# Kernel tuning notes

Hardware: AMD Instinct MI355X
Metric: run time of the kernel (lower is better)

## Reference

```python
import jax, jax.numpy as jnp
import numpy as np

N_NODES = 50000
N_EDGES = 500000
IN_DIM = 128
HIDDEN = 32
HEADS = 8
OUT_DIM = HIDDEN * HEADS  # 256
NEG_SLOPE = 0.2


def setup_inputs() -> dict:
    key = jax.random.key(0)
    ks = jax.random.split(key, 10)
    s = lambda fan: 1.0 / np.sqrt(fan)
    x = jax.random.normal(ks[0], (N_NODES, IN_DIM), dtype=jnp.float32)
    edge_index = jax.random.randint(ks[1], (2, N_EDGES), 0, N_NODES, dtype=jnp.int32)
    W1 = jax.random.normal(ks[2], (IN_DIM, HEADS * HIDDEN), jnp.float32) * s(IN_DIM)
    a_src1 = jax.random.normal(ks[3], (HEADS, HIDDEN), jnp.float32) * s(HIDDEN)
    a_dst1 = jax.random.normal(ks[4], (HEADS, HIDDEN), jnp.float32) * s(HIDDEN)
    b1 = jnp.zeros((HEADS * HIDDEN,), jnp.float32)
    W2 = jax.random.normal(ks[5], (OUT_DIM, OUT_DIM), jnp.float32) * s(OUT_DIM)
    a_src2 = jax.random.normal(ks[6], (1, OUT_DIM), jnp.float32) * s(OUT_DIM)
    a_dst2 = jax.random.normal(ks[7], (1, OUT_DIM), jnp.float32) * s(OUT_DIM)
    b2 = jnp.zeros((OUT_DIM,), jnp.float32)
    return {"x": x, "edge_index": edge_index, "W1": W1, "a_src1": a_src1,
            "a_dst1": a_dst1, "b1": b1, "W2": W2, "a_src2": a_src2,
            "a_dst2": a_dst2, "b2": b2}


def _gat_layer(x, src, dst, W, a_src, a_dst, b, heads, ch, concat):
    N = x.shape[0]
    h = (x @ W).reshape(N, heads, ch)                      # [N,H,C]
    e_src = jnp.sum(h * a_src[None], axis=-1)              # [N,H]
    e_dst = jnp.sum(h * a_dst[None], axis=-1)              # [N,H]
    e = jax.nn.leaky_relu(e_src[src] + e_dst[dst], NEG_SLOPE)  # [E,H]
    # softmax over incoming edges of each destination node
    m = jax.ops.segment_max(e, dst, num_segments=N)        # [N,H]
    e = jnp.exp(e - m[dst])
    denom = jax.ops.segment_sum(e, dst, num_segments=N)    # [N,H]
    alpha = e / (denom[dst] + 1e-16)                       # [E,H]
    msg = h[src] * alpha[:, :, None]                       # [E,H,C]
    out = jax.ops.segment_sum(msg, dst, num_segments=N)    # [N,H,C]
    out = out.reshape(N, heads * ch) if concat else out.mean(axis=1)
    return out + b


def reference(x, edge_index, W1, a_src1, a_dst1, b1, W2, a_src2, a_dst2, b2):
    N = x.shape[0]
    # add self loops (PyG GATConv default)
    loops = jnp.arange(N, dtype=edge_index.dtype)
    src = jnp.concatenate([edge_index[0], loops])
    dst = jnp.concatenate([edge_index[1], loops])
    # dropout is identity in eval mode
    h = _gat_layer(x, src, dst, W1, a_src1, a_dst1, b1, HEADS, HIDDEN, True)
    h = jax.nn.elu(h)
    out = _gat_layer(h, src, dst, W2, a_src2, a_dst2, b2, 1, OUT_DIM, False)
    return out
```

## Files before the change

kernel.cpp:

```cpp
#include <hip/hip_runtime.h>
#include <math.h>

#define N_NODES 50000
#define E_ORIG  500000
#define E_TOT   550000
#define NB      196

typedef _Float16 half8 __attribute__((ext_vector_type(8)));
typedef _Float16 half4 __attribute__((ext_vector_type(4)));
typedef float    v4f   __attribute__((ext_vector_type(4)));

__global__ void k_zero(int* __restrict__ p, int n) {
    int i = blockIdx.x * blockDim.x + threadIdx.x;
    if (i < n) p[i] = 0;
}

__global__ void k_count(const int* __restrict__ ei, int* __restrict__ deg) {
    int e = blockIdx.x * blockDim.x + threadIdx.x;
    if (e >= E_TOT) return;
    int d = (e < E_ORIG) ? ei[E_ORIG + e] : (e - E_ORIG);
    atomicAdd(&deg[d], 1);
}

__global__ __launch_bounds__(256) void k_blocksum(const int* __restrict__ deg,
                                                  int* __restrict__ bsum) {
    int t = threadIdx.x;
    int i = blockIdx.x * 256 + t;
    int v = (i < N_NODES) ? deg[i] : 0;
#pragma unroll
    for (int mk = 1; mk < 64; mk <<= 1) v += __shfl_xor(v, mk, 64);
    __shared__ int ws[4];
    if ((t & 63) == 0) ws[t >> 6] = v;
    __syncthreads();
    if (t == 0) bsum[blockIdx.x] = ws[0] + ws[1] + ws[2] + ws[3];
}

__global__ __launch_bounds__(256) void k_scanbsum(const int* __restrict__ bsum,
                                                  int* __restrict__ boff) {
    __shared__ int s[256];
    int t = threadIdx.x;
    int v = (t < NB) ? bsum[t] : 0;
    s[t] = v;
    __syncthreads();
    for (int o = 1; o < 256; o <<= 1) {
        int x = (t >= o) ? s[t - o] : 0;
        __syncthreads();
        s[t] += x;
        __syncthreads();
    }
    if (t <= NB) boff[t] = (t == 0) ? 0 : s[t - 1];
}

__global__ __launch_bounds__(256) void k_offsets(const int* __restrict__ deg,
                                                 const int* __restrict__ boff,
                                                 int* __restrict__ offsets,
                                                 int* __restrict__ cur) {
    __shared__ int s[256];
    int t = threadIdx.x;
    int i = blockIdx.x * 256 + t;
    int v = (i < N_NODES) ? deg[i] : 0;
    s[t] = v;
    __syncthreads();
    for (int o = 1; o < 256; o <<= 1) {
        int x = (t >= o) ? s[t - o] : 0;
        __syncthreads();
        s[t] += x;
        __syncthreads();
    }
    int off = boff[blockIdx.x] + s[t] - v;
    if (i <= N_NODES) {
        offsets[i] = off;
        if (i < N_NODES) cur[i] = off;
    }
}

__global__ void k_scatter(const int* __restrict__ ei, int* __restrict__ cur,
                          int* __restrict__ csr_src) {
    int e = blockIdx.x * blockDim.x + threadIdx.x;
    if (e >= E_TOT) return;
    int s, d;
    if (e < E_ORIG) { s = ei[e]; d = ei[E_ORIG + e]; }
    else            { s = e - E_ORIG; d = s; }
    int slot = atomicAdd(&cur[d], 1);
    csr_src[slot] = s;
}

__global__ void k_prepw(const float* __restrict__ W1, const float* __restrict__ W2,
                        const float* __restrict__ as2, const float* __restrict__ ad2,
                        _Float16* __restrict__ w1t, _Float16* __restrict__ w2t,
                        float* __restrict__ vs2, float* __restrict__ vd2) {
    int i = blockIdx.x * blockDim.x + threadIdx.x;
    if (i < 128 * 256) {
        int k = i >> 8, c = i & 255;
        w1t[(size_t)c * 128 + k] = (_Float16)W1[i];
        return;
    }
    int j = i - 128 * 256;
    if (j < 256 * 256) {
        int k = j >> 8, c = j & 255;
        w2t[(size_t)c * 256 + k] = (_Float16)W2[j];
        return;
    }
    int k = j - 256 * 256;
    if (k < 256) {
        float s = 0.f, d = 0.f;
        for (int c = 0; c < 256; c++) {
            float w = W2[(size_t)k * 256 + c];
            s += w * as2[c];
            d += w * ad2[c];
        }
        vs2[k] = s;
        vd2[k] = d;
    }
}

__global__ __launch_bounds__(256) void k_gemm1(
    const float* __restrict__ X, const _Float16* __restrict__ Bt,
    const float* __restrict__ a_s, const float* __restrict__ a_d,
    _Float16* __restrict__ H, float* __restrict__ es, float* __restrict__ ed) {
    int t = threadIdx.x, w = t >> 6, lane = t & 63;
    int quad = lane >> 4, l16 = lane & 15;
    int row0 = blockIdx.x * 32;
    int colbase = w * 64;

    v4f acc[2][4];
#pragma unroll
    for (int i = 0; i < 2; i++)
#pragma unroll
        for (int j = 0; j < 4; j++) acc[i][j] = (v4f){0.f, 0.f, 0.f, 0.f};

    int r0 = row0 + l16;      if (r0 >= N_NODES) r0 = N_NODES - 1;
    int r1 = row0 + 16 + l16; if (r1 >= N_NODES) r1 = N_NODES - 1;
    const float4* a0p = (const float4*)(X + (size_t)r0 * 128) + quad * 2;
    const float4* a1p = (const float4*)(X + (size_t)r1 * 128) + quad * 2;
    const half8* bp[4];
#pragma unroll
    for (int ct = 0; ct < 4; ct++)
        bp[ct] = (const half8*)(Bt + (size_t)(colbase + ct * 16 + l16) * 128 + quad * 8);

#pragma unroll
    for (int kc = 0; kc < 4; kc++) {
        float4 f0 = a0p[kc * 8], f1 = a0p[kc * 8 + 1];
        float4 f2 = a1p[kc * 8], f3 = a1p[kc * 8 + 1];
        half8 av0 = (half8){(_Float16)f0.x, (_Float16)f0.y, (_Float16)f0.z, (_Float16)f0.w,
                            (_Float16)f1.x, (_Float16)f1.y, (_Float16)f1.z, (_Float16)f1.w};
        half8 av1 = (half8){(_Float16)f2.x, (_Float16)f2.y, (_Float16)f2.z, (_Float16)f2.w,
                            (_Float16)f3.x, (_Float16)f3.y, (_Float16)f3.z, (_Float16)f3.w};
#pragma unroll
        for (int ct = 0; ct < 4; ct++) {
            half8 bv = bp[ct][kc * 4];
            acc[0][ct] = __builtin_amdgcn_mfma_f32_16x16x32_f16(av0, bv, acc[0][ct], 0, 0, 0);
            acc[1][ct] = __builtin_amdgcn_mfma_f32_16x16x32_f16(av1, bv, acc[1][ct], 0, 0, 0);
        }
    }

    float asv[4], adv[4];
#pragma unroll
    for (int ct = 0; ct < 4; ct++) {
        asv[ct] = a_s[colbase + ct * 16 + l16];
        adv[ct] = a_d[colbase + ct * 16 + l16];
    }
#pragma unroll
    for (int rt = 0; rt < 2; rt++) {
#pragma unroll
        for (int hp = 0; hp < 2; hp++) {
#pragma unroll
            for (int reg = 0; reg < 4; reg++) {
                float ps = acc[rt][2 * hp][reg] * asv[2 * hp] +
                           acc[rt][2 * hp + 1][reg] * asv[2 * hp + 1];
                float pd = acc[rt][2 * hp][reg] * adv[2 * hp] +
                           acc[rt][2 * hp + 1][reg] * adv[2 * hp + 1];
#pragma unroll
                for (int mk = 1; mk < 16; mk <<= 1) {
                    ps += __shfl_xor(ps, mk, 64);
                    pd += __shfl_xor(pd, mk, 64);
                }
                if (l16 == 0) {
                    int row = row0 + rt * 16 + quad * 4 + reg;
                    if (row < N_NODES) {
                        int head = w * 2 + hp;
                        es[(size_t)row * 8 + head] = ps;
                        ed[(size_t)row * 8 + head] = pd;
                    }
                }
            }
        }
    }

    __shared__ _Float16 SH[32][264];
#pragma unroll
    for (int rt = 0; rt < 2; rt++)
#pragma unroll
        for (int ct = 0; ct < 4; ct++)
#pragma unroll
            for (int reg = 0; reg < 4; reg++)
                SH[rt * 16 + quad * 4 + reg][colbase + ct * 16 + l16] =
                    (_Float16)acc[rt][ct][reg];
    __syncthreads();
#pragma unroll
    for (int j = 0; j < 4; j++) {
        int c = j * 256 + t;
        int row = c >> 5, col8 = c & 31;
        int gr = row0 + row;
        if (gr < N_NODES)
            *(half8*)(H + (size_t)gr * 256 + col8 * 8) = *(const half8*)&SH[row][col8 * 8];
    }
}

__global__ __launch_bounds__(256) void k_gemm2(
    const _Float16* __restrict__ A, const _Float16* __restrict__ Bt,
    const float* __restrict__ bias, float* __restrict__ OUT) {
    int t = threadIdx.x, w = t >> 6, lane = t & 63;
    int quad = lane >> 4, l16 = lane & 15;
    int row0 = blockIdx.x * 32;
    int colbase = w * 64;

    v4f acc[2][4];
#pragma unroll
    for (int i = 0; i < 2; i++)
#pragma unroll
        for (int j = 0; j < 4; j++) acc[i][j] = (v4f){0.f, 0.f, 0.f, 0.f};

    int r0 = row0 + l16;      if (r0 >= N_NODES) r0 = N_NODES - 1;
    int r1 = row0 + 16 + l16; if (r1 >= N_NODES) r1 = N_NODES - 1;
    const half8* a0 = (const half8*)(A + (size_t)r0 * 256 + quad * 8);
    const half8* a1 = (const half8*)(A + (size_t)r1 * 256 + quad * 8);
    const half8* bp[4];
#pragma unroll
    for (int ct = 0; ct < 4; ct++)
        bp[ct] = (const half8*)(Bt + (size_t)(colbase + ct * 16 + l16) * 256 + quad * 8);

#pragma unroll
    for (int kc = 0; kc < 8; kc++) {
        half8 av0 = a0[kc * 4];
        half8 av1 = a1[kc * 4];
#pragma unroll
        for (int ct = 0; ct < 4; ct++) {
            half8 bv = bp[ct][kc * 4];
            acc[0][ct] = __builtin_amdgcn_mfma_f32_16x16x32_f16(av0, bv, acc[0][ct], 0, 0, 0);
            acc[1][ct] = __builtin_amdgcn_mfma_f32_16x16x32_f16(av1, bv, acc[1][ct], 0, 0, 0);
        }
    }

    __shared__ float SF[32][260];
#pragma unroll
    for (int rt = 0; rt < 2; rt++)
#pragma unroll
        for (int ct = 0; ct < 4; ct++)
#pragma unroll
            for (int reg = 0; reg < 4; reg++)
                SF[rt * 16 + quad * 4 + reg][colbase + ct * 16 + l16] = acc[rt][ct][reg];
    __syncthreads();
#pragma unroll
    for (int j = 0; j < 8; j++) {
        int c = j * 256 + t;
        int row = c >> 6, c4 = c & 63;
        int gr = row0 + row;
        if (gr < N_NODES) {
            float4 v = *(const float4*)&SF[row][c4 * 4];
            float4 bb = ((const float4*)bias)[c4];
            float4 o = make_float4(v.x + bb.x, v.y + bb.y, v.z + bb.z, v.w + bb.w);
            *(float4*)(OUT + (size_t)gr * 256 + c4 * 4) = o;
        }
    }
}

__global__ __launch_bounds__(256) void k_agg1(
    const _Float16* __restrict__ H1, const float* __restrict__ es,
    const float* __restrict__ ed, const int* __restrict__ offsets,
    const int* __restrict__ csr_src, const float* __restrict__ b1,
    const float* __restrict__ vs2, const float* __restrict__ vd2,
    _Float16* __restrict__ out1, float* __restrict__ es2,
    float* __restrict__ ed2) {
    int t = threadIdx.x, w = t >> 6, lane = t & 63;
    int n = blockIdx.x * 4 + w;
    int hB = lane >> 3;
    int beg = offsets[n];
    int deg = offsets[n + 1] - beg;
    float edl = ed[(size_t)n * 8 + hB];

    const half4* __restrict__ Hl = (const half4*)H1 + lane;
    float a0 = 0.f, a1 = 0.f, a2 = 0.f, a3 = 0.f, den = 0.f;

    for (int base = 0; base < deg; base += 64) {
        int rem = deg - base; if (rem > 64) rem = 64;
        int idx = beg + base + lane;
        if (idx >= E_TOT) idx = E_TOT - 1;
        int sreg = csr_src[idx];
        int i = 0;
        for (; i + 1 < rem; i += 2) {
            int s0 = __shfl(sreg, i);
            int s1 = __shfl(sreg, i + 1);
            float l0 = es[(size_t)s0 * 8 + hB] + edl;
            float l1 = es[(size_t)s1 * 8 + hB] + edl;
            l0 = l0 > 0.f ? l0 : 0.2f * l0;
            l1 = l1 > 0.f ? l1 : 0.2f * l1;
            float w0 = __expf(l0), w1 = __expf(l1);
            half4 h0 = Hl[(size_t)s0 * 64];
            half4 h1 = Hl[(size_t)s1 * 64];
            a0 += w0 * (float)h0[0]; a1 += w0 * (float)h0[1];
            a2 += w0 * (float)h0[2]; a3 += w0 * (float)h0[3];
            a0 += w1 * (float)h1[0]; a1 += w1 * (float)h1[1];
            a2 += w1 * (float)h1[2]; a3 += w1 * (float)h1[3];
            den += w0 + w1;
        }
        if (i < rem) {
            int s0 = __shfl(sreg, i);
            float l0 = es[(size_t)s0 * 8 + hB] + edl;
            l0 = l0 > 0.f ? l0 : 0.2f * l0;
            float w0 = __expf(l0);
            half4 h0 = Hl[(size_t)s0 * 64];
            a0 += w0 * (float)h0[0]; a1 += w0 * (float)h0[1];
            a2 += w0 * (float)h0[2]; a3 += w0 * (float)h0[3];
            den += w0;
        }
    }

    float r = 1.f / (den + 1e-16f);
    float4 bb = ((const float4*)b1)[lane];
    float o0 = a0 * r + bb.x, o1 = a1 * r + bb.y;
    float o2 = a2 * r + bb.z, o3 = a3 * r + bb.w;
    o0 = o0 > 0.f ? o0 : __expf(o0) - 1.f;
    o1 = o1 > 0.f ? o1 : __expf(o1) - 1.f;
    o2 = o2 > 0.f ? o2 : __expf(o2) - 1.f;
    o3 = o3 > 0.f ? o3 : __expf(o3) - 1.f;
    ((half4*)(out1 + (size_t)n * 256))[lane] =
        (half4){(_Float16)o0, (_Float16)o1, (_Float16)o2, (_Float16)o3};

    float4 vs = ((const float4*)vs2)[lane];
    float4 vd = ((const float4*)vd2)[lane];
    float ps = o0 * vs.x + o1 * vs.y + o2 * vs.z + o3 * vs.w;
    float pd = o0 * vd.x + o1 * vd.y + o2 * vd.z + o3 * vd.w;
#pragma unroll
    for (int mk = 1; mk < 64; mk <<= 1) {
        ps += __shfl_xor(ps, mk, 64);
        pd += __shfl_xor(pd, mk, 64);
    }
    if (lane == 0) { es2[n] = ps; ed2[n] = pd; }
}

__global__ __launch_bounds__(256) void k_agg2(
    const _Float16* __restrict__ O1, const float* __restrict__ es2,
    const float* __restrict__ ed2, const int* __restrict__ offsets,
    const int* __restrict__ csr_src, _Float16* __restrict__ xagg) {
    int t = threadIdx.x, w = t >> 6, lane = t & 63;
    int n = blockIdx.x * 4 + w;
    int beg = offsets[n];
    int deg = offsets[n + 1] - beg;
    float edn = ed2[n];

    const half4* __restrict__ Ol = (const half4*)O1 + lane;
    float a0 = 0.f, a1 = 0.f, a2 = 0.f, a3 = 0.f, den = 0.f;

    for (int base = 0; base < deg; base += 64) {
        int rem = deg - base; if (rem > 64) rem = 64;
        int idx = beg + base + lane;
        if (idx >= E_TOT) idx = E_TOT - 1;
        int sreg = csr_src[idx];
        int i = 0;
        for (; i + 1 < rem; i += 2) {
            int s0 = __shfl(sreg, i);
            int s1 = __shfl(sreg, i + 1);
            float l0 = es2[s0] + edn;
            float l1 = es2[s1] + edn;
            l0 = l0 > 0.f ? l0 : 0.2f * l0;
            l1 = l1 > 0.f ? l1 : 0.2f * l1;
            float w0 = __expf(l0), w1 = __expf(l1);
            half4 h0 = Ol[(size_t)s0 * 64];
            half4 h1 = Ol[(size_t)s1 * 64];
            a0 += w0 * (float)h0[0]; a1 += w0 * (float)h0[1];
            a2 += w0 * (float)h0[2]; a3 += w0 * (float)h0[3];
            a0 += w1 * (float)h1[0]; a1 += w1 * (float)h1[1];
            a2 += w1 * (float)h1[2]; a3 += w1 * (float)h1[3];
            den += w0 + w1;
        }
        if (i < rem) {
            int s0 = __shfl(sreg, i);
            float l0 = es2[s0] + edn;
            l0 = l0 > 0.f ? l0 : 0.2f * l0;
            float w0 = __expf(l0);
            half4 h0 = Ol[(size_t)s0 * 64];
            a0 += w0 * (float)h0[0]; a1 += w0 * (float)h0[1];
            a2 += w0 * (float)h0[2]; a3 += w0 * (float)h0[3];
            den += w0;
        }
    }

    float r = 1.f / (den + 1e-16f);
    ((half4*)(xagg + (size_t)n * 256))[lane] =
        (half4){(_Float16)(a0 * r), (_Float16)(a1 * r),
                (_Float16)(a2 * r), (_Float16)(a3 * r)};
}

extern "C" void kernel_launch(void* const* d_in, const int* in_sizes, int n_in,
                              void* d_out, int out_size, void* d_ws, size_t ws_size,
                              hipStream_t stream) {
    const float* x   = (const float*)d_in[0];
    const int*   ei  = (const int*)d_in[1];
    const float* W1  = (const float*)d_in[2];
    const float* as1 = (const float*)d_in[3];
    const float* ad1 = (const float*)d_in[4];
    const float* b1  = (const float*)d_in[5];
    const float* W2  = (const float*)d_in[6];
    const float* as2 = (const float*)d_in[7];
    const float* ad2 = (const float*)d_in[8];
    const float* b2  = (const float*)d_in[9];
    float* out = (float*)d_out;

    char* ws = (char*)d_ws;
    size_t off = 0;
    auto alloc = [&](size_t bytes) {
        void* p = ws + off;
        off = (off + bytes + 255) & ~(size_t)255;
        return p;
    };
    _Float16* h1h     = (_Float16*)alloc((size_t)N_NODES * 256 * 2);
    _Float16* out1h   = (_Float16*)alloc((size_t)N_NODES * 256 * 2);
    _Float16* xagg    = (_Float16*)alloc((size_t)N_NODES * 256 * 2);
    _Float16* w1t     = (_Float16*)alloc((size_t)128 * 256 * 2);
    _Float16* w2t     = (_Float16*)alloc((size_t)256 * 256 * 2);
    float*    es1     = (float*)alloc((size_t)N_NODES * 8 * 4);
    float*    ed1     = (float*)alloc((size_t)N_NODES * 8 * 4);
    float*    es2     = (float*)alloc((size_t)N_NODES * 4);
    float*    ed2     = (float*)alloc((size_t)N_NODES * 4);
    float*    vs2     = (float*)alloc(256 * 4);
    float*    vd2     = (float*)alloc(256 * 4);
    int*      deg     = (int*)alloc((size_t)N_NODES * 4);
    int*      offsets = (int*)alloc((size_t)(N_NODES + 1) * 4);
    int*      cur     = (int*)alloc((size_t)N_NODES * 4);
    int*      csr_src = (int*)alloc((size_t)E_TOT * 4);
    int*      bsum    = (int*)alloc((size_t)NB * 4);
    int*      boff    = (int*)alloc((size_t)(NB + 1) * 4);

    const int TB = 256;
    int gridN = (N_NODES + TB - 1) / TB;
    int gridE = (E_TOT + TB - 1) / TB;
    int gridG = (N_NODES + 31) / 32;
    int gridA = N_NODES / 4;

    k_zero<<<gridN, TB, 0, stream>>>(deg, N_NODES);
    k_count<<<gridE, TB, 0, stream>>>(ei, deg);
    k_blocksum<<<NB, TB, 0, stream>>>(deg, bsum);
    k_scanbsum<<<1, TB, 0, stream>>>(bsum, boff);
    k_offsets<<<NB, TB, 0, stream>>>(deg, boff, offsets, cur);
    k_scatter<<<gridE, TB, 0, stream>>>(ei, cur, csr_src);

    int prepN = 128 * 256 + 256 * 256 + 256;
    k_prepw<<<(prepN + TB - 1) / TB, TB, 0, stream>>>(W1, W2, as2, ad2,
                                                      w1t, w2t, vs2, vd2);

    k_gemm1<<<gridG, TB, 0, stream>>>(x, w1t, as1, ad1, h1h, es1, ed1);
    k_agg1<<<gridA, TB, 0, stream>>>(h1h, es1, ed1, offsets, csr_src, b1,
                                     vs2, vd2, out1h, es2, ed2);

    k_agg2<<<gridA, TB, 0, stream>>>(out1h, es2, ed2, offsets, csr_src, xagg);
    k_gemm2<<<gridG, TB, 0, stream>>>(xagg, w2t, b2, out);
}
```

Baseline: 329.0 us.

## Fuse degree count into weight prep, halve GEMM LDS staging, unroll aggregation by four

```diff
diff --git a/kernel.cpp b/kernel.cpp
--- a/kernel.cpp
+++ b/kernel.cpp
@@ -10,16 +10,41 @@
 typedef _Float16 half4 __attribute__((ext_vector_type(4)));
 typedef float    v4f   __attribute__((ext_vector_type(4)));
 
-__global__ void k_zero(int* __restrict__ p, int n) {
+__global__ void k_prepw(const float* __restrict__ W1, const float* __restrict__ W2,
+                        const float* __restrict__ as2, const float* __restrict__ ad2,
+                        const int* __restrict__ ei,
+                        _Float16* __restrict__ w1t, _Float16* __restrict__ w2t,
+                        float* __restrict__ vs2, float* __restrict__ vd2,
+                        int* __restrict__ deg) {
     int i = blockIdx.x * blockDim.x + threadIdx.x;
-    if (i < n) p[i] = 0;
-}
-
-__global__ void k_count(const int* __restrict__ ei, int* __restrict__ deg) {
-    int e = blockIdx.x * blockDim.x + threadIdx.x;
-    if (e >= E_TOT) return;
-    int d = (e < E_ORIG) ? ei[E_ORIG + e] : (e - E_ORIG);
-    atomicAdd(&deg[d], 1);
+    if (i < E_TOT) {
+        int d = (i < E_ORIG) ? ei[E_ORIG + i] : (i - E_ORIG);
+        atomicAdd(&deg[d], 1);
+        return;
+    }
+    int j = i - E_TOT;
+    if (j < 128 * 256) {
+        int k = j >> 8, c = j & 255;
+        w1t[(size_t)c * 128 + k] = (_Float16)W1[j];
+        return;
+    }
+    j -= 128 * 256;
+    if (j < 256 * 256) {
+        int k = j >> 8, c = j & 255;
+        w2t[(size_t)c * 256 + k] = (_Float16)W2[j];
+        return;
+    }
+    j -= 256 * 256;
+    if (j < 256) {
+        float s = 0.f, d = 0.f;
+        for (int c = 0; c < 256; c++) {
+            float w = W2[(size_t)j * 256 + c];
+            s += w * as2[c];
+            d += w * ad2[c];
+        }
+        vs2[j] = s;
+        vd2[j] = d;
+    }
 }
 
 __global__ __launch_bounds__(256) void k_blocksum(const int* __restrict__ deg,
@@ -83,35 +108,6 @@
     else            { s = e - E_ORIG; d = s; }
     int slot = atomicAdd(&cur[d], 1);
     csr_src[slot] = s;
-}
-
-__global__ void k_prepw(const float* __restrict__ W1, const float* __restrict__ W2,
-                        const float* __restrict__ as2, const float* __restrict__ ad2,
-                        _Float16* __restrict__ w1t, _Float16* __restrict__ w2t,
-                        float* __restrict__ vs2, float* __restrict__ vd2) {
-    int i = blockIdx.x * blockDim.x + threadIdx.x;
-    if (i < 128 * 256) {
-        int k = i >> 8, c = i & 255;
-        w1t[(size_t)c * 128 + k] = (_Float16)W1[i];
-        return;
-    }
-    int j = i - 128 * 256;
-    if (j < 256 * 256) {
-        int k = j >> 8, c = j & 255;
-        w2t[(size_t)c * 256 + k] = (_Float16)W2[j];
-        return;
-    }
-    int k = j - 256 * 256;
-    if (k < 256) {
-        float s = 0.f, d = 0.f;
-        for (int c = 0; c < 256; c++) {
-            float w = W2[(size_t)k * 256 + c];
-            s += w * as2[c];
-            d += w * ad2[c];
-        }
-        vs2[k] = s;
-        vd2[k] = d;
-    }
 }
 
 __global__ __launch_bounds__(256) void k_gemm1(
@@ -187,23 +183,24 @@
         }
     }
 
-    __shared__ _Float16 SH[32][264];
-#pragma unroll
-    for (int rt = 0; rt < 2; rt++)
+    __shared__ _Float16 SH[16][264];
+#pragma unroll
+    for (int rt = 0; rt < 2; rt++) {
+        if (rt) __syncthreads();
 #pragma unroll
         for (int ct = 0; ct < 4; ct++)
 #pragma unroll
             for (int reg = 0; reg < 4; reg++)
-                SH[rt * 16 + quad * 4 + reg][colbase + ct * 16 + l16] =
-                    (_Float16)acc[rt][ct][reg];
-    __syncthreads();
-#pragma unroll
-    for (int j = 0; j < 4; j++) {
-        int c = j * 256 + t;
-        int row = c >> 5, col8 = c & 31;
-        int gr = row0 + row;
-        if (gr < N_NODES)
-            *(half8*)(H + (size_t)gr * 256 + col8 * 8) = *(const half8*)&SH[row][col8 * 8];
+                SH[quad * 4 + reg][colbase + ct * 16 + l16] = (_Float16)acc[rt][ct][reg];
+        __syncthreads();
+#pragma unroll
+        for (int j = 0; j < 2; j++) {
+            int c = j * 256 + t;
+            int row = c >> 5, col8 = c & 31;
+            int gr = row0 + rt * 16 + row;
+            if (gr < N_NODES)
+                *(half8*)(H + (size_t)gr * 256 + col8 * 8) = *(const half8*)&SH[row][col8 * 8];
+        }
     }
 }
 
@@ -242,25 +239,27 @@
         }
     }
 
-    __shared__ float SF[32][260];
-#pragma unroll
-    for (int rt = 0; rt < 2; rt++)
+    __shared__ float SF[16][260];
+#pragma unroll
+    for (int rt = 0; rt < 2; rt++) {
+        if (rt) __syncthreads();
 #pragma unroll
         for (int ct = 0; ct < 4; ct++)
 #pragma unroll
             for (int reg = 0; reg < 4; reg++)
-                SF[rt * 16 + quad * 4 + reg][colbase + ct * 16 + l16] = acc[rt][ct][reg];
-    __syncthreads();
-#pragma unroll
-    for (int j = 0; j < 8; j++) {
-        int c = j * 256 + t;
-        int row = c >> 6, c4 = c & 63;
-        int gr = row0 + row;
-        if (gr < N_NODES) {
-            float4 v = *(const float4*)&SF[row][c4 * 4];
-            float4 bb = ((const float4*)bias)[c4];
-            float4 o = make_float4(v.x + bb.x, v.y + bb.y, v.z + bb.z, v.w + bb.w);
-            *(float4*)(OUT + (size_t)gr * 256 + c4 * 4) = o;
+                SF[quad * 4 + reg][colbase + ct * 16 + l16] = acc[rt][ct][reg];
+        __syncthreads();
+#pragma unroll
+        for (int j = 0; j < 4; j++) {
+            int c = j * 256 + t;
+            int row = c >> 6, c4 = c & 63;
+            int gr = row0 + rt * 16 + row;
+            if (gr < N_NODES) {
+                float4 v = *(const float4*)&SF[row][c4 * 4];
+                float4 bb = ((const float4*)bias)[c4];
+                float4 o = make_float4(v.x + bb.x, v.y + bb.y, v.z + bb.z, v.w + bb.w);
+                *(float4*)(OUT + (size_t)gr * 256 + c4 * 4) = o;
+            }
         }
     }
 }
@@ -279,7 +278,8 @@
     int deg = offsets[n + 1] - beg;
     float edl = ed[(size_t)n * 8 + hB];
 
-    const half4* __restrict__ Hl = (const half4*)H1 + lane;
+    const char* __restrict__ Hb  = (const char*)H1 + lane * 8;
+    const char* __restrict__ esb = (const char*)es + hB * 4;
     float a0 = 0.f, a1 = 0.f, a2 = 0.f, a3 = 0.f, den = 0.f;
 
     for (int base = 0; base < deg; base += 64) {
@@ -288,28 +288,39 @@
         if (idx >= E_TOT) idx = E_TOT - 1;
         int sreg = csr_src[idx];
         int i = 0;
-        for (; i + 1 < rem; i += 2) {
-            int s0 = __shfl(sreg, i);
-            int s1 = __shfl(sreg, i + 1);
-            float l0 = es[(size_t)s0 * 8 + hB] + edl;
-            float l1 = es[(size_t)s1 * 8 + hB] + edl;
+        for (; i + 3 < rem; i += 4) {
+            int s0 = __shfl(sreg, i), s1 = __shfl(sreg, i + 1);
+            int s2 = __shfl(sreg, i + 2), s3 = __shfl(sreg, i + 3);
+            float l0 = *(const float*)(esb + ((unsigned)s0 << 5)) + edl;
+            float l1 = *(const float*)(esb + ((unsigned)s1 << 5)) + edl;
+            float l2 = *(const float*)(esb + ((unsigned)s2 << 5)) + edl;
+            float l3 = *(const float*)(esb + ((unsigned)s3 << 5)) + edl;
+            half4 h0 = *(const half4*)(Hb + ((unsigned)s0 << 9));
+            half4 h1 = *(const half4*)(Hb + ((unsigned)s1 << 9));
+            half4 h2 = *(const half4*)(Hb + ((unsigned)s2 << 9));
+            half4 h3 = *(const half4*)(Hb + ((unsigned)s3 << 9));
             l0 = l0 > 0.f ? l0 : 0.2f * l0;
             l1 = l1 > 0.f ? l1 : 0.2f * l1;
+            l2 = l2 > 0.f ? l2 : 0.2f * l2;
+            l3 = l3 > 0.f ? l3 : 0.2f * l3;
             float w0 = __expf(l0), w1 = __expf(l1);
-            half4 h0 = Hl[(size_t)s0 * 64];
-            half4 h1 = Hl[(size_t)s1 * 64];
+            float w2 = __expf(l2), w3 = __expf(l3);
             a0 += w0 * (float)h0[0]; a1 += w0 * (float)h0[1];
             a2 += w0 * (float)h0[2]; a3 += w0 * (float)h0[3];
             a0 += w1 * (float)h1[0]; a1 += w1 * (float)h1[1];
             a2 += w1 * (float)h1[2]; a3 += w1 * (float)h1[3];
-            den += w0 + w1;
-        }
-        if (i < rem) {
+            a0 += w2 * (float)h2[0]; a1 += w2 * (float)h2[1];
+            a2 += w2 * (float)h2[2]; a3 += w2 * (float)h2[3];
+            a0 += w3 * (float)h3[0]; a1 += w3 * (float)h3[1];
+            a2 += w3 * (float)h3[2]; a3 += w3 * (float)h3[3];
+            den += w0 + w1 + w2 + w3;
+        }
+        for (; i < rem; i++) {
             int s0 = __shfl(sreg, i);
-            float l0 = es[(size_t)s0 * 8 + hB] + edl;
+            float l0 = *(const float*)(esb + ((unsigned)s0 << 5)) + edl;
             l0 = l0 > 0.f ? l0 : 0.2f * l0;
             float w0 = __expf(l0);
-            half4 h0 = Hl[(size_t)s0 * 64];
+            half4 h0 = *(const half4*)(Hb + ((unsigned)s0 << 9));
             a0 += w0 * (float)h0[0]; a1 += w0 * (float)h0[1];
             a2 += w0 * (float)h0[2]; a3 += w0 * (float)h0[3];
             den += w0;
@@ -349,7 +360,8 @@
     int deg = offsets[n + 1] - beg;
     float edn = ed2[n];
 
-    const half4* __restrict__ Ol = (const half4*)O1 + lane;
+    const char* __restrict__ Ob  = (const char*)O1 + lane * 8;
+    const char* __restrict__ eb  = (const char*)es2;
     float a0 = 0.f, a1 = 0.f, a2 = 0.f, a3 = 0.f, den = 0.f;
 
     for (int base = 0; base < deg; base += 64) {
@@ -358,28 +370,39 @@
         if (idx >= E_TOT) idx = E_TOT - 1;
         int sreg = csr_src[idx];
         int i = 0;
-        for (; i + 1 < rem; i += 2) {
-            int s0 = __shfl(sreg, i);
-            int s1 = __shfl(sreg, i + 1);
-            float l0 = es2[s0] + edn;
-            float l1 = es2[s1] + edn;
+        for (; i + 3 < rem; i += 4) {
+            int s0 = __shfl(sreg, i), s1 = __shfl(sreg, i + 1);
+            int s2 = __shfl(sreg, i + 2), s3 = __shfl(sreg, i + 3);
+            float l0 = *(const float*)(eb + ((unsigned)s0 << 2)) + edn;
+            float l1 = *(const float*)(eb + ((unsigned)s1 << 2)) + edn;
+            float l2 = *(const float*)(eb + ((unsigned)s2 << 2)) + edn;
+            float l3 = *(const float*)(eb + ((unsigned)s3 << 2)) + edn;
+            half4 h0 = *(const half4*)(Ob + ((unsigned)s0 << 9));
+            half4 h1 = *(const half4*)(Ob + ((unsigned)s1 << 9));
+            half4 h2 = *(const half4*)(Ob + ((unsigned)s2 << 9));
+            half4 h3 = *(const half4*)(Ob + ((unsigned)s3 << 9));
             l0 = l0 > 0.f ? l0 : 0.2f * l0;
             l1 = l1 > 0.f ? l1 : 0.2f * l1;
+            l2 = l2 > 0.f ? l2 : 0.2f * l2;
+            l3 = l3 > 0.f ? l3 : 0.2f * l3;
             float w0 = __expf(l0), w1 = __expf(l1);
-            half4 h0 = Ol[(size_t)s0 * 64];
-            half4 h1 = Ol[(size_t)s1 * 64];
+            float w2 = __expf(l2), w3 = __expf(l3);
             a0 += w0 * (float)h0[0]; a1 += w0 * (float)h0[1];
             a2 += w0 * (float)h0[2]; a3 += w0 * (float)h0[3];
             a0 += w1 * (float)h1[0]; a1 += w1 * (float)h1[1];
             a2 += w1 * (float)h1[2]; a3 += w1 * (float)h1[3];
-            den += w0 + w1;
-        }
-        if (i < rem) {
+            a0 += w2 * (float)h2[0]; a1 += w2 * (float)h2[1];
+            a2 += w2 * (float)h2[2]; a3 += w2 * (float)h2[3];
+            a0 += w3 * (float)h3[0]; a1 += w3 * (float)h3[1];
+            a2 += w3 * (float)h3[2]; a3 += w3 * (float)h3[3];
+            den += w0 + w1 + w2 + w3;
+        }
+        for (; i < rem; i++) {
             int s0 = __shfl(sreg, i);
-            float l0 = es2[s0] + edn;
+            float l0 = *(const float*)(eb + ((unsigned)s0 << 2)) + edn;
             l0 = l0 > 0.f ? l0 : 0.2f * l0;
             float w0 = __expf(l0);
-            half4 h0 = Ol[(size_t)s0 * 64];
+            half4 h0 = *(const half4*)(Ob + ((unsigned)s0 << 9));
             a0 += w0 * (float)h0[0]; a1 += w0 * (float)h0[1];
             a2 += w0 * (float)h0[2]; a3 += w0 * (float)h0[3];
             den += w0;
@@ -433,22 +456,19 @@
     int*      boff    = (int*)alloc((size_t)(NB + 1) * 4);
 
     const int TB = 256;
-    int gridN = (N_NODES + TB - 1) / TB;
     int gridE = (E_TOT + TB - 1) / TB;
     int gridG = (N_NODES + 31) / 32;
     int gridA = N_NODES / 4;
 
-    k_zero<<<gridN, TB, 0, stream>>>(deg, N_NODES);
-    k_count<<<gridE, TB, 0, stream>>>(ei, deg);
+    hipMemsetAsync(deg, 0, (size_t)N_NODES * 4, stream);
+    int prepN = E_TOT + 128 * 256 + 256 * 256 + 256;
+    k_prepw<<<(prepN + TB - 1) / TB, TB, 0, stream>>>(W1, W2, as2, ad2, ei,
+                                                      w1t, w2t, vs2, vd2, deg);
     k_blocksum<<<NB, TB, 0, stream>>>(deg, bsum);
     k_scanbsum<<<1, TB, 0, stream>>>(bsum, boff);
     k_offsets<<<NB, TB, 0, stream>>>(deg, boff, offsets, cur);
     k_scatter<<<gridE, TB, 0, stream>>>(ei, cur, csr_src);
 
-    int prepN = 128 * 256 + 256 * 256 + 256;
-    k_prepw<<<(prepN + TB - 1) / TB, TB, 0, stream>>>(W1, W2, as2, ad2,
-                                                      w1t, w2t, vs2, vd2);
-
     k_gemm1<<<gridG, TB, 0, stream>>>(x, w1t, as1, ad1, h1h, es1, ed1);
     k_agg1<<<gridA, TB, 0, stream>>>(h1h, es1, ed1, offsets, csr_src, b1,
                                      vs2, vd2, out1h, es2, ed2);
```

Measured after the change: 320.0 us. -2.7%, faster.
